# Performance work log

Hardware: AMD Instinct MI355X
Metric: run time of the kernel (lower is better)

The kernel has to match this reference:

```python
import jax, jax.numpy as jnp
import numpy as np

N_NODES = 100000
N_EDGES = 1600000
IN_F = 128
C1, C2, C3 = 32, 64, 64
HEADS, GAT_CH = 4, 16  # concat -> 64
NEG_SLOPE = 0.2  # PyG GATConv default leaky_relu slope


def _add_self_loops(src, dst, n):
    loop = jnp.arange(n, dtype=src.dtype)
    return jnp.concatenate([src, loop]), jnp.concatenate([dst, loop])


def gcn_conv(x, src, dst, W, b, n):
    # PyG GCNConv: D^{-1/2} (A + I) D^{-1/2} X W + b  (self-loops already in src/dst)
    h = x @ W
    deg = jax.ops.segment_sum(jnp.ones_like(dst, dtype=h.dtype), dst, num_segments=n)
    dinv = jnp.where(deg > 0, jax.lax.rsqrt(deg), 0.0)
    norm = dinv[src] * dinv[dst]                              # [E]
    out = jax.ops.segment_sum(h[src] * norm[:, None], dst, num_segments=n)
    return out + b


def gat_conv(x, src, dst, W, att_src, att_dst, b, n):
    # PyG GATConv (concat=True), self-loops already in src/dst
    h = (x @ W).reshape(n, HEADS, GAT_CH)                     # [N,H,C]
    a_s = jnp.sum(h * att_src, axis=-1)                       # [N,H]
    a_d = jnp.sum(h * att_dst, axis=-1)                       # [N,H]
    e = jax.nn.leaky_relu(a_s[src] + a_d[dst], NEG_SLOPE)     # [E,H]
    # segment softmax over incoming edges of each dst node
    emax = jax.ops.segment_max(e, dst, num_segments=n)
    ex = jnp.exp(e - emax[dst])
    denom = jax.ops.segment_sum(ex, dst, num_segments=n)
    alpha = ex / (denom[dst] + 1e-16)                         # [E,H]
    out = jax.ops.segment_sum(h[src] * alpha[:, :, None], dst, num_segments=n)
    return out.reshape(n, HEADS * GAT_CH) + b


def setup_inputs() -> dict:
    key = jax.random.key(0)
    ks = jax.random.split(key, 16)
    x = jax.random.normal(ks[0], (N_NODES, IN_F), dtype=jnp.float32)
    edge_index = jax.random.randint(ks[1], (2, N_EDGES), 0, N_NODES, dtype=jnp.int32)
    s = 0.1
    return {
        "x": x,
        "edge_index": edge_index,
        "W1": jax.random.normal(ks[2], (IN_F, C1), jnp.float32) * s,
        "b1": jnp.zeros((C1,), jnp.float32),
        "W2": jax.random.normal(ks[3], (C1, C2), jnp.float32) * s,
        "b2": jnp.zeros((C2,), jnp.float32),
        "W3": jax.random.normal(ks[4], (C3, C3), jnp.float32) * s,
        "b3": jnp.zeros((C3,), jnp.float32),
        "Wg": jax.random.normal(ks[5], (C2, HEADS * GAT_CH), jnp.float32) * s,
        "att_src": jax.random.normal(ks[6], (HEADS, GAT_CH), jnp.float32) * s,
        "att_dst": jax.random.normal(ks[7], (HEADS, GAT_CH), jnp.float32) * s,
        "bg": jnp.zeros((HEADS * GAT_CH,), jnp.float32),
        "Wl": jax.random.normal(ks[8], (HEADS * GAT_CH, 1), jnp.float32) * s,
        "bl": jnp.zeros((1,), jnp.float32),
    }


def reference(x, edge_index, W1, b1, W2, b2, W3, b3, Wg, att_src, att_dst, bg, Wl, bl):
    n = x.shape[0]
    src, dst = _add_self_loops(edge_index[0], edge_index[1], n)
    h = jax.nn.relu(gcn_conv(x, src, dst, W1, b1, n))           # dropout = identity (eval)
    h = jax.nn.relu(gcn_conv(h, src, dst, W2, b2, n))
    h = jax.nn.relu(gat_conv(h, src, dst, Wg, att_src, att_dst, bg, n))
    h_res = jax.nn.relu(gcn_conv(h, src, dst, W3, b3, n))
    h = h + h_res
    h = jax.nn.relu(gat_conv(h, src, dst, Wg, att_src, att_dst, bg, n))
    return jax.nn.relu(h @ Wl + bl)                              # [N,1]
```

## Files before the change

kernel.cpp:

```cpp
#include <hip/hip_runtime.h>
#include <math.h>

constexpr int KIN = 128;

typedef _Float16 half8_t __attribute__((ext_vector_type(8)));
typedef _Float16 half4_t __attribute__((ext_vector_type(4)));


__global__ void rx_hist(const int* __restrict__ dst, int* __restrict__ hist_g,
                        int E, int CH, int NB, int NBKT) {
    __shared__ int h[256];
    int b = blockIdx.x;
    for (int i = threadIdx.x; i < 256; i += blockDim.x) h[i] = 0;
    __syncthreads();
    int beg = b * CH, end = min(beg + CH, E);
    for (int e = beg + threadIdx.x; e < end; e += blockDim.x)
        atomicAdd(&h[dst[e] >> 9], 1);
    __syncthreads();
    for (int d = threadIdx.x; d < NBKT; d += blockDim.x)
        hist_g[d * NB + b] = h[d];
}

__global__ void gs_reduce(const int* __restrict__ a, int* __restrict__ bsum, int m) {
    __shared__ int s[256];
    int t = threadIdx.x;
    int i = blockIdx.x * 256 + t;
    s[t] = (i < m) ? a[i] : 0;
    __syncthreads();
    for (int off = 128; off > 0; off >>= 1) {
        if (t < off) s[t] += s[t + off];
        __syncthreads();
    }
    if (t == 0) bsum[blockIdx.x] = s[0];
}

__global__ void gs_blocksums(const int* __restrict__ bsum, int* __restrict__ bpre, int nb) {
    __shared__ int s[512];
    int t = threadIdx.x;
    int val = (t < nb) ? bsum[t] : 0;
    s[t] = val;
    __syncthreads();
    for (int off = 1; off < 512; off <<= 1) {
        int x = (t >= off) ? s[t - off] : 0;
        __syncthreads();
        s[t] += x;
        __syncthreads();
    }
    if (t < nb) bpre[t] = s[t] - val;
}

__global__ void gs_scatter(const int* __restrict__ a, const int* __restrict__ bpre,
                           int* __restrict__ out, int m) {
    __shared__ int s[256];
    int t = threadIdx.x;
    int i = blockIdx.x * 256 + t;
    int val = (i < m) ? a[i] : 0;
    s[t] = val;
    __syncthreads();
    for (int off = 1; off < 256; off <<= 1) {
        int x = (t >= off) ? s[t - off] : 0;
        __syncthreads();
        s[t] += x;
        __syncthreads();
    }
    if (i < m) out[i] = bpre[blockIdx.x] + s[t] - val;
}

__global__ void rx_scatter(const int* __restrict__ src, const int* __restrict__ dst,
                           const int* __restrict__ excl, int* __restrict__ s1,
                           int* __restrict__ d1, int E, int CH, int NB, int NBKT) {
    __shared__ int offs[256];
    int b = blockIdx.x;
    for (int d = threadIdx.x; d < NBKT; d += blockDim.x)
        offs[d] = excl[d * NB + b];
    __syncthreads();
    int beg = b * CH, end = min(beg + CH, E);
    for (int e = beg + threadIdx.x; e < end; e += blockDim.x) {
        int dd = dst[e];
        int pos = atomicAdd(&offs[dd >> 9], 1);
        s1[pos] = src[e];
        d1[pos] = dd;
    }
}

__global__ void __launch_bounds__(512)
bucket_sort(const int* __restrict__ s1, const int* __restrict__ d1,
            const int* __restrict__ excl, int* __restrict__ csr,
            int* __restrict__ row_ptr, float* __restrict__ dinv,
            int E, int NB, int NBKT, int n) {
    __shared__ int hist[512];
    __shared__ int scan[512];
    __shared__ int offs[512];
    int b = blockIdx.x, t = threadIdx.x;
    int base = excl[b * NB];
    int endb = (b + 1 < NBKT) ? excl[(b + 1) * NB] : E;
    hist[t] = 0;
    __syncthreads();
    for (int i = base + t; i < endb; i += 512)
        atomicAdd(&hist[d1[i] & 511], 1);
    __syncthreads();
    int v = hist[t];
    scan[t] = v;
    __syncthreads();
    for (int off = 1; off < 512; off <<= 1) {
        int x = (t >= off) ? scan[t - off] : 0;
        __syncthreads();
        scan[t] += x;
        __syncthreads();
    }
    int ex = scan[t] - v;
    offs[t] = ex;
    int node = b * 512 + t;
    if (node < n) {
        row_ptr[node] = base + ex;
        dinv[node] = 1.0f / sqrtf((float)(v + 1));
    }
    if (b == NBKT - 1 && t == 0) row_ptr[n] = E;
    __syncthreads();
    for (int i = base + t; i < endb; i += 512) {
        int dd = d1[i];
        int pos = atomicAdd(&offs[dd & 511], 1);
        csr[base + pos] = s1[i];
    }
}

template <int K, int F, int BM, int THREADS, bool SCALE, bool BRELU, bool ATT, bool OUT16>
__global__ void __launch_bounds__(THREADS)
gemm_tile(const float* __restrict__ in, const float* __restrict__ W,
          const float* __restrict__ dinv, const float* __restrict__ bias,
          const float* __restrict__ att_src, const float* __restrict__ att_dst,
          float* __restrict__ a_s, float* __restrict__ a_d,
          float* __restrict__ out, int n) {
    constexpr int TM = 4, TN = 4;
    constexpr int TX = F / TN;
    constexpr int TY = BM / TM;
    static_assert(THREADS == TX * TY, "thread count mismatch");
    constexpr int K4 = K / 4;
    __shared__ float xs[K][BM];
    __shared__ float Ws[K * F];
    int t = threadIdx.x;
    int row0 = blockIdx.x * BM;

    for (int i = t; i < K * F / 4; i += THREADS)
        ((float4*)Ws)[i] = ((const float4*)W)[i];

    for (int i = t; i < BM * K4; i += THREADS) {
        int r = i % BM, k4 = i / BM;
        int row = row0 + r;
        float4 v = {0.f, 0.f, 0.f, 0.f};
        if (row < n) v = ((const float4*)(in + (size_t)row * K))[k4];
        xs[4 * k4 + 0][r] = v.x;
        xs[4 * k4 + 1][r] = v.y;
        xs[4 * k4 + 2][r] = v.z;
        xs[4 * k4 + 3][r] = v.w;
    }
    __syncthreads();

    int tx = t % TX, ty = t / TX;
    float acc[TM][TN] = {};
#pragma unroll 4
    for (int k = 0; k < K; ++k) {
        float4 xv = *(const float4*)&xs[k][ty * TM];
        float4 wv = *(const float4*)&Ws[k * F + tx * TN];
        float xr[4] = {xv.x, xv.y, xv.z, xv.w};
        float wr[4] = {wv.x, wv.y, wv.z, wv.w};
#pragma unroll
        for (int i = 0; i < TM; ++i)
#pragma unroll
            for (int j = 0; j < TN; ++j)
                acc[i][j] = fmaf(xr[i], wr[j], acc[i][j]);
    }

#pragma unroll
    for (int i = 0; i < TM; ++i) {
        int row = row0 + ty * TM + i;
        if (row >= n) continue;
        float s = SCALE ? dinv[row] : 1.0f;
        float o[4];
        if (BRELU) {
            o[0] = fmaxf(fmaf(acc[i][0], s, bias[4 * tx + 0]), 0.f);
            o[1] = fmaxf(fmaf(acc[i][1], s, bias[4 * tx + 1]), 0.f);
            o[2] = fmaxf(fmaf(acc[i][2], s, bias[4 * tx + 2]), 0.f);
            o[3] = fmaxf(fmaf(acc[i][3], s, bias[4 * tx + 3]), 0.f);
        } else {
            o[0] = acc[i][0] * s; o[1] = acc[i][1] * s;
            o[2] = acc[i][2] * s; o[3] = acc[i][3] * s;
        }
        if (OUT16) {
            half4_t oh;
            oh[0] = (_Float16)o[0]; oh[1] = (_Float16)o[1];
            oh[2] = (_Float16)o[2]; oh[3] = (_Float16)o[3];
            *(half4_t*)((_Float16*)out + (size_t)row * F + 4 * tx) = oh;
        } else {
            float4 of = {o[0], o[1], o[2], o[3]};
            ((float4*)(out + (size_t)row * F))[tx] = of;
        }
    }
    if (ATT) {
        int hd = tx >> 2;
        float as0 = att_src[4 * tx + 0], as1 = att_src[4 * tx + 1];
        float as2 = att_src[4 * tx + 2], as3 = att_src[4 * tx + 3];
        float ad0 = att_dst[4 * tx + 0], ad1 = att_dst[4 * tx + 1];
        float ad2 = att_dst[4 * tx + 2], ad3 = att_dst[4 * tx + 3];
#pragma unroll
        for (int i = 0; i < TM; ++i) {
            float ps = acc[i][0] * as0 + acc[i][1] * as1 + acc[i][2] * as2 + acc[i][3] * as3;
            float pd = acc[i][0] * ad0 + acc[i][1] * ad1 + acc[i][2] * ad2 + acc[i][3] * ad3;
            ps += __shfl_xor(ps, 1); pd += __shfl_xor(pd, 1);
            ps += __shfl_xor(ps, 2); pd += __shfl_xor(pd, 2);
            int row = row0 + ty * TM + i;
            if ((tx & 3) == 0 && row < n) {
                a_s[row * 4 + hd] = ps;
                a_d[row * 4 + hd] = pd;
            }
        }
    }
}

__global__ void __launch_bounds__(256)
gemm2_gat(const float* __restrict__ T, const float* __restrict__ W2,
          const float* __restrict__ b2, const float* __restrict__ dinv,
          const float* __restrict__ Wg, const float* __restrict__ att_src,
          const float* __restrict__ att_dst, float* __restrict__ a_s,
          float* __restrict__ a_d, float* __restrict__ A1, int n) {
    __shared__ float xs[32][64];
    __shared__ float W2s[32 * 64];
    __shared__ float Wgs[64 * 64];
    __shared__ float hs[64][68];
    int t = threadIdx.x;
    int row0 = blockIdx.x * 64;

    for (int i = t; i < 32 * 64 / 4; i += 256) ((float4*)W2s)[i] = ((const float4*)W2)[i];
    for (int i = t; i < 64 * 64 / 4; i += 256) ((float4*)Wgs)[i] = ((const float4*)Wg)[i];
    for (int i = t; i < 64 * 8; i += 256) {
        int r = i % 64, k4 = i / 64;
        int row = row0 + r;
        float4 v = {0.f, 0.f, 0.f, 0.f};
        if (row < n) v = ((const float4*)(T + (size_t)row * 32))[k4];
        xs[4 * k4 + 0][r] = v.x;
        xs[4 * k4 + 1][r] = v.y;
        xs[4 * k4 + 2][r] = v.z;
        xs[4 * k4 + 3][r] = v.w;
    }
    __syncthreads();

    int tx = t % 16, ty = t / 16;
    {
        float acc[4][4] = {};
#pragma unroll 4
        for (int k = 0; k < 32; ++k) {
            float4 xv = *(const float4*)&xs[k][ty * 4];
            float4 wv = *(const float4*)&W2s[k * 64 + tx * 4];
            float xr[4] = {xv.x, xv.y, xv.z, xv.w};
            float wr[4] = {wv.x, wv.y, wv.z, wv.w};
#pragma unroll
            for (int i = 0; i < 4; ++i)
#pragma unroll
                for (int j = 0; j < 4; ++j)
                    acc[i][j] = fmaf(xr[i], wr[j], acc[i][j]);
        }
#pragma unroll
        for (int i = 0; i < 4; ++i) {
            int row = row0 + ty * 4 + i;
            float s = (row < n) ? dinv[row] : 0.f;
#pragma unroll
            for (int j = 0; j < 4; ++j)
                hs[4 * tx + j][ty * 4 + i] = fmaxf(fmaf(acc[i][j], s, b2[4 * tx + j]), 0.f);
        }
    }
    __syncthreads();

    float acc[4][4] = {};
#pragma unroll 4
    for (int k = 0; k < 64; ++k) {
        float4 xv = *(const float4*)&hs[k][ty * 4];
        float4 wv = *(const float4*)&Wgs[k * 64 + tx * 4];
        float xr[4] = {xv.x, xv.y, xv.z, xv.w};
        float wr[4] = {wv.x, wv.y, wv.z, wv.w};
#pragma unroll
        for (int i = 0; i < 4; ++i)
#pragma unroll
            for (int j = 0; j < 4; ++j)
                acc[i][j] = fmaf(xr[i], wr[j], acc[i][j]);
    }
    _Float16* A1h = (_Float16*)A1;
#pragma unroll
    for (int i = 0; i < 4; ++i) {
        int row = row0 + ty * 4 + i;
        if (row >= n) continue;
        half4_t oh;
        oh[0] = (_Float16)acc[i][0]; oh[1] = (_Float16)acc[i][1];
        oh[2] = (_Float16)acc[i][2]; oh[3] = (_Float16)acc[i][3];
        *(half4_t*)(A1h + (size_t)row * 64 + 4 * tx) = oh;
    }
    {
        int hd = tx >> 2;
        float as0 = att_src[4 * tx + 0], as1 = att_src[4 * tx + 1];
        float as2 = att_src[4 * tx + 2], as3 = att_src[4 * tx + 3];
        float ad0 = att_dst[4 * tx + 0], ad1 = att_dst[4 * tx + 1];
        float ad2 = att_dst[4 * tx + 2], ad3 = att_dst[4 * tx + 3];
#pragma unroll
        for (int i = 0; i < 4; ++i) {
            float ps = acc[i][0] * as0 + acc[i][1] * as1 + acc[i][2] * as2 + acc[i][3] * as3;
            float pd = acc[i][0] * ad0 + acc[i][1] * ad1 + acc[i][2] * ad2 + acc[i][3] * ad3;
            ps += __shfl_xor(ps, 1); pd += __shfl_xor(pd, 1);
            ps += __shfl_xor(ps, 2); pd += __shfl_xor(pd, 2);
            int row = row0 + ty * 4 + i;
            if ((tx & 3) == 0 && row < n) {
                a_s[row * 4 + hd] = ps;
                a_d[row * 4 + hd] = pd;
            }
        }
    }
}

template <int F, int MODE, bool RES>
__global__ void gcn_agg_w(const float* __restrict__ Hs, const int* __restrict__ row_ptr,
                          const int* __restrict__ csr, const float* __restrict__ dinv,
                          const float* __restrict__ bias, const float* __restrict__ res,
                          float* __restrict__ out, int n) {
    constexpr int CG = F / 4;
    constexpr int SLOTS = 64 / CG;
    int idx = blockIdx.x * blockDim.x + threadIdx.x;
    int v = idx >> 6;
    int lane = idx & 63;
    if (v >= n) return;
    int cg = lane % CG;
    int slot = lane / CG;
    const float4* H4 = (const float4*)Hs;

    float4 acc = {0.f, 0.f, 0.f, 0.f};
    if (slot == 0) acc = H4[(size_t)v * CG + cg];

    int beg = row_ptr[v], end = row_ptr[v + 1];
    int iters = (end - beg + SLOTS - 1) / SLOTS;
    int e = beg + slot;
    bool val = e < end;
    int u = val ? csr[e] : v;
    float4 h = H4[(size_t)u * CG + cg];
    for (int i = 0; i < iters; ++i) {
        int en = e + SLOTS;
        bool valn = en < end;
        int un = valn ? csr[en] : v;
        float4 hn = H4[(size_t)un * CG + cg];
        float m = val ? 1.f : 0.f;
        acc.x = fmaf(m, h.x, acc.x);
        acc.y = fmaf(m, h.y, acc.y);
        acc.z = fmaf(m, h.z, acc.z);
        acc.w = fmaf(m, h.w, acc.w);
        e = en; val = valn; h = hn;
    }
    for (int off = CG; off < 64; off <<= 1) {
        acc.x += __shfl_xor(acc.x, off);
        acc.y += __shfl_xor(acc.y, off);
        acc.z += __shfl_xor(acc.z, off);
        acc.w += __shfl_xor(acc.w, off);
    }
    if (slot == 0) {
        float4 o;
        if (MODE == 2) {
            o = acc;
        } else {
            float dv = dinv[v];
            o.x = fmaxf(fmaf(dv, acc.x, bias[4 * cg + 0]), 0.f);
            o.y = fmaxf(fmaf(dv, acc.y, bias[4 * cg + 1]), 0.f);
            o.z = fmaxf(fmaf(dv, acc.z, bias[4 * cg + 2]), 0.f);
            o.w = fmaxf(fmaf(dv, acc.w, bias[4 * cg + 3]), 0.f);
            if (MODE == 1) { o.x *= dv; o.y *= dv; o.z *= dv; o.w *= dv; }
            if (RES) {
                const float4 r = ((const float4*)res)[(size_t)v * CG + cg];
                o.x += r.x; o.y += r.y; o.z += r.z; o.w += r.w;
            }
        }
        ((float4*)out)[(size_t)v * CG + cg] = o;
    }
}

__global__ void __launch_bounds__(256)
gcn_agg_h64(const _Float16* __restrict__ Hs, const int* __restrict__ row_ptr,
            const int* __restrict__ csr, const float* __restrict__ dinv,
            const float* __restrict__ bias, const float* __restrict__ res,
            float* __restrict__ out, int n) {
    int idx = blockIdx.x * blockDim.x + threadIdx.x;
    int v = idx >> 6;
    int lane = idx & 63;
    if (v >= n) return;
    int cg = lane & 7;
    int slot = lane >> 3;
    const half8_t* H8 = (const half8_t*)Hs;

    float acc[8] = {};
    if (slot == 0) {
        half8_t h = H8[(size_t)v * 8 + cg];
#pragma unroll
        for (int j = 0; j < 8; ++j) acc[j] = (float)h[j];
    }
    int beg = row_ptr[v], end = row_ptr[v + 1];
    int iters = (end - beg + 7) >> 3;
    int e = beg + slot;
    bool val = e < end;
    int u = val ? csr[e] : v;
    half8_t h = H8[(size_t)u * 8 + cg];
    for (int i = 0; i < iters; ++i) {
        int en = e + 8;
        bool valn = en < end;
        int un = valn ? csr[en] : v;
        half8_t hn = H8[(size_t)un * 8 + cg];
        float m = val ? 1.f : 0.f;
#pragma unroll
        for (int j = 0; j < 8; ++j) acc[j] = fmaf(m, (float)h[j], acc[j]);
        e = en; val = valn; h = hn;
    }
#pragma unroll
    for (int off = 8; off < 64; off <<= 1) {
#pragma unroll
        for (int j = 0; j < 8; ++j) acc[j] += __shfl_xor(acc[j], off);
    }
    if (slot == 0) {
        float dv = dinv[v];
        const float4* r4 = (const float4*)(res + (size_t)v * 64 + 8 * cg);
        float4 r0 = r4[0], r1 = r4[1];
        float o[8];
#pragma unroll
        for (int j = 0; j < 8; ++j)
            o[j] = fmaxf(fmaf(dv, acc[j], bias[8 * cg + j]), 0.f);
        float4 o0 = {o[0] + r0.x, o[1] + r0.y, o[2] + r0.z, o[3] + r0.w};
        float4 o1 = {o[4] + r1.x, o[5] + r1.y, o[6] + r1.z, o[7] + r1.w};
        float4* dst4 = (float4*)(out + (size_t)v * 64 + 8 * cg);
        dst4[0] = o0;
        dst4[1] = o1;
    }
}

template <bool FINAL>
__global__ void __launch_bounds__(256)
gat_agg_h(const _Float16* __restrict__ H, const int* __restrict__ row_ptr,
          const int* __restrict__ csr, const float* __restrict__ a_s,
          const float* __restrict__ a_d, const float* __restrict__ bias,
          const float* __restrict__ Wl, const float* __restrict__ bl,
          float* __restrict__ out, int n) {
    int idx = blockIdx.x * blockDim.x + threadIdx.x;
    int v = idx >> 6;
    int lane = idx & 63;
    if (v >= n) return;
    int cg = lane & 7;
    int slot = lane >> 3;
    int hd = cg >> 1;
    const half8_t* H8 = (const half8_t*)H;

    float adv = a_d[v * 4 + hd];
    float l = 0.f;
    float acc[8] = {};
    if (slot == 0) {
        float e0 = a_s[v * 4 + hd] + adv;
        e0 = (e0 >= 0.f) ? e0 : 0.2f * e0;
        float p = __expf(e0);
        l = p;
        half8_t h = H8[(size_t)v * 8 + cg];
#pragma unroll
        for (int j = 0; j < 8; ++j) acc[j] = p * (float)h[j];
    }
    int beg = row_ptr[v], end = row_ptr[v + 1];
    int iters = (end - beg + 7) >> 3;
    int e = beg + slot;
    bool val = e < end;
    int u = val ? csr[e] : v;
    half8_t h = H8[(size_t)u * 8 + cg];
    float as = a_s[u * 4 + hd];
    for (int i = 0; i < iters; ++i) {
        int en = e + 8;
        bool valn = en < end;
        int un = valn ? csr[en] : v;
        half8_t hn = H8[(size_t)un * 8 + cg];
        float asn = a_s[un * 4 + hd];
        float ev = as + adv;
        ev = (ev >= 0.f) ? ev : 0.2f * ev;
        float p = val ? __expf(ev) : 0.f;
        l += p;
#pragma unroll
        for (int j = 0; j < 8; ++j) acc[j] = fmaf(p, (float)h[j], acc[j]);
        e = en; val = valn; h = hn; as = asn;
    }
#pragma unroll
    for (int off = 8; off < 64; off <<= 1) {
        l += __shfl_xor(l, off);
#pragma unroll
        for (int j = 0; j < 8; ++j) acc[j] += __shfl_xor(acc[j], off);
    }
    float rl = 1.0f / (l + 1e-16f);
    if (!FINAL) {
        if (slot == 0) {
            float o[8];
#pragma unroll
            for (int j = 0; j < 8; ++j)
                o[j] = fmaxf(fmaf(acc[j], rl, bias[8 * cg + j]), 0.f);
            float4 o0 = {o[0], o[1], o[2], o[3]};
            float4 o1 = {o[4], o[5], o[6], o[7]};
            float4* dst4 = (float4*)(out + (size_t)v * 64 + 8 * cg);
            dst4[0] = o0;
            dst4[1] = o1;
        }
    } else {
        float p = 0.f;
#pragma unroll
        for (int j = 0; j < 8; ++j)
            p += fmaxf(fmaf(acc[j], rl, bias[8 * cg + j]), 0.f) * Wl[8 * cg + j];
        p += __shfl_xor(p, 1);
        p += __shfl_xor(p, 2);
        p += __shfl_xor(p, 4);
        if (lane == 0) out[v] = fmaxf(p + bl[0], 0.f);
    }
}


extern "C" void kernel_launch(void* const* d_in, const int* in_sizes, int n_in,
                              void* d_out, int out_size, void* d_ws, size_t ws_size,
                              hipStream_t stream) {
    const float* x     = (const float*)d_in[0];
    const int*   ei    = (const int*)d_in[1];
    const float* W1    = (const float*)d_in[2];
    const float* b1    = (const float*)d_in[3];
    const float* W2    = (const float*)d_in[4];
    const float* b2    = (const float*)d_in[5];
    const float* W3    = (const float*)d_in[6];
    const float* b3    = (const float*)d_in[7];
    const float* Wg    = (const float*)d_in[8];
    const float* att_s = (const float*)d_in[9];
    const float* att_d = (const float*)d_in[10];
    const float* bg    = (const float*)d_in[11];
    const float* Wl    = (const float*)d_in[12];
    const float* bl    = (const float*)d_in[13];
    float* out = (float*)d_out;

    int n = in_sizes[0] / KIN;
    int E = in_sizes[1] / 2;
    const int* srcp = ei;
    const int* dstp = ei + E;

    int NB = 128;
    int CH = (E + NB - 1) / NB;
    int NBKT = (n + 511) >> 9;
    int M = NBKT * NB;

    char* w = (char*)d_ws;
    auto alloc = [&](size_t bytes) -> void* {
        void* p = (void*)w;
        w += (bytes + 255) & ~(size_t)255;
        return p;
    };
    int*   row_ptr = (int*)alloc((size_t)(n + 1) * 4);
    int*   csr     = (int*)alloc((size_t)E * 4);
    int*   hist_g  = (int*)alloc((size_t)M * 4);
    int*   excl    = (int*)alloc((size_t)M * 4);
    int*   bsum    = (int*)alloc(512 * 4);
    int*   bpre    = (int*)alloc(512 * 4);
    float* dinv    = (float*)alloc((size_t)n * 4);
    float* a_s     = (float*)alloc((size_t)n * 4 * 4);
    float* a_d     = (float*)alloc((size_t)n * 4 * 4);
    float* bufA    = (float*)alloc((size_t)n * 64 * 4);
    float* bufB    = (float*)alloc((size_t)n * 64 * 4);
    float* bufC    = (float*)alloc((size_t)n * 64 * 4);
    int* s1 = (int*)bufB;
    int* d1 = ((int*)bufB) + E;

    int msb = (M + 255) / 256;
    rx_hist<<<NB, 256, 0, stream>>>(dstp, hist_g, E, CH, NB, NBKT);
    gs_reduce<<<msb, 256, 0, stream>>>(hist_g, bsum, M);
    gs_blocksums<<<1, 512, 0, stream>>>(bsum, bpre, msb);
    gs_scatter<<<msb, 256, 0, stream>>>(hist_g, bpre, excl, M);
    rx_scatter<<<NB, 256, 0, stream>>>(srcp, dstp, excl, s1, d1, E, CH, NB, NBKT);
    bucket_sort<<<NBKT, 512, 0, stream>>>(s1, d1, excl, csr, row_ptr, dinv, E, NB, NBKT, n);

    int agg_blocks = (n * 64 + 255) / 256;
    int gemm_blocks = (n + 63) / 64;

    gemm_tile<128, 32, 64, 128, true, false, false, false><<<gemm_blocks, 128, 0, stream>>>(
        x, W1, dinv, nullptr, nullptr, nullptr, nullptr, nullptr, bufA, n);
    gcn_agg_w<32, 1, false><<<agg_blocks, 256, 0, stream>>>(bufA, row_ptr, csr, dinv, b1, nullptr, bufB, n);
    gcn_agg_w<32, 2, false><<<agg_blocks, 256, 0, stream>>>(bufB, row_ptr, csr, nullptr, nullptr, nullptr, bufA, n);
    gemm2_gat<<<gemm_blocks, 256, 0, stream>>>(bufA, W2, b2, dinv, Wg, att_s, att_d, a_s, a_d, bufB, n);
    gat_agg_h<false><<<agg_blocks, 256, 0, stream>>>(
        (const _Float16*)bufB, row_ptr, csr, a_s, a_d, bg, nullptr, nullptr, bufC, n);
    gemm_tile<64, 64, 64, 256, true, false, false, true><<<gemm_blocks, 256, 0, stream>>>(
        bufC, W3, dinv, nullptr, nullptr, nullptr, nullptr, nullptr, bufA, n);
    gcn_agg_h64<<<agg_blocks, 256, 0, stream>>>(
        (const _Float16*)bufA, row_ptr, csr, dinv, b3, bufC, bufB, n);
    gemm_tile<64, 64, 64, 256, false, false, true, true><<<gemm_blocks, 256, 0, stream>>>(
        bufB, Wg, nullptr, nullptr, att_s, att_d, a_s, a_d, bufA, n);
    gat_agg_h<true><<<agg_blocks, 256, 0, stream>>>(
        (const _Float16*)bufA, row_ptr, csr, a_s, a_d, bg, Wl, bl, out, n);
}
```

Baseline: 508.8 us.

## Store first GCN layer features in fp16 and widen GAT per-lane head work

The first GEMM now writes fp16 output, and both 32-wide GCN aggregations gather fp16 rows using 16 edge slots per wavefront instead of 8. The middle aggregation also emits fp16 for the next one. This halves gather bytes in the first layer. Separately, the GAT aggregation gives each lane a whole head (16 channels), so 16 edges are processed in parallel per node instead of 8, at the cost of more registers and shuffles per lane. fp16 intermediates add rounding error.

```diff
diff --git a/kernel.cpp b/kernel.cpp
--- a/kernel.cpp
+++ b/kernel.cpp
@@ -314,65 +314,62 @@
     }
 }
 
-template <int F, int MODE, bool RES>
-__global__ void gcn_agg_w(const float* __restrict__ Hs, const int* __restrict__ row_ptr,
-                          const int* __restrict__ csr, const float* __restrict__ dinv,
-                          const float* __restrict__ bias, const float* __restrict__ res,
-                          float* __restrict__ out, int n) {
-    constexpr int CG = F / 4;
-    constexpr int SLOTS = 64 / CG;
+template <int MODE>
+__global__ void __launch_bounds__(256)
+gcn_agg_h32(const _Float16* __restrict__ Hs, const int* __restrict__ row_ptr,
+            const int* __restrict__ csr, const float* __restrict__ dinv,
+            const float* __restrict__ bias, void* __restrict__ outp, int n) {
     int idx = blockIdx.x * blockDim.x + threadIdx.x;
     int v = idx >> 6;
     int lane = idx & 63;
     if (v >= n) return;
-    int cg = lane % CG;
-    int slot = lane / CG;
-    const float4* H4 = (const float4*)Hs;
-
-    float4 acc = {0.f, 0.f, 0.f, 0.f};
-    if (slot == 0) acc = H4[(size_t)v * CG + cg];
-
+    int cg = lane & 3;
+    int slot = lane >> 2;
+    const half8_t* H8 = (const half8_t*)Hs;
+
+    float acc[8] = {};
+    if (slot == 0) {
+        half8_t h = H8[(size_t)v * 4 + cg];
+#pragma unroll
+        for (int j = 0; j < 8; ++j) acc[j] = (float)h[j];
+    }
     int beg = row_ptr[v], end = row_ptr[v + 1];
-    int iters = (end - beg + SLOTS - 1) / SLOTS;
+    int iters = (end - beg + 15) >> 4;
     int e = beg + slot;
     bool val = e < end;
     int u = val ? csr[e] : v;
-    float4 h = H4[(size_t)u * CG + cg];
+    half8_t h = H8[(size_t)u * 4 + cg];
     for (int i = 0; i < iters; ++i) {
-        int en = e + SLOTS;
+        int en = e + 16;
         bool valn = en < end;
         int un = valn ? csr[en] : v;
-        float4 hn = H4[(size_t)un * CG + cg];
+        half8_t hn = H8[(size_t)un * 4 + cg];
         float m = val ? 1.f : 0.f;
-        acc.x = fmaf(m, h.x, acc.x);
-        acc.y = fmaf(m, h.y, acc.y);
-        acc.z = fmaf(m, h.z, acc.z);
-        acc.w = fmaf(m, h.w, acc.w);
+#pragma unroll
+        for (int j = 0; j < 8; ++j) acc[j] = fmaf(m, (float)h[j], acc[j]);
         e = en; val = valn; h = hn;
     }
-    for (int off = CG; off < 64; off <<= 1) {
-        acc.x += __shfl_xor(acc.x, off);
-        acc.y += __shfl_xor(acc.y, off);
-        acc.z += __shfl_xor(acc.z, off);
-        acc.w += __shfl_xor(acc.w, off);
+#pragma unroll
+    for (int off = 4; off < 64; off <<= 1) {
+#pragma unroll
+        for (int j = 0; j < 8; ++j) acc[j] += __shfl_xor(acc[j], off);
     }
     if (slot == 0) {
-        float4 o;
-        if (MODE == 2) {
-            o = acc;
+        if (MODE == 1) {
+            float dv = dinv[v];
+            half8_t o;
+#pragma unroll
+            for (int j = 0; j < 8; ++j)
+                o[j] = (_Float16)(dv * fmaxf(fmaf(dv, acc[j], bias[8 * cg + j]), 0.f));
+            ((half8_t*)outp)[(size_t)v * 4 + cg] = o;
         } else {
-            float dv = dinv[v];
-            o.x = fmaxf(fmaf(dv, acc.x, bias[4 * cg + 0]), 0.f);
-            o.y = fmaxf(fmaf(dv, acc.y, bias[4 * cg + 1]), 0.f);
-            o.z = fmaxf(fmaf(dv, acc.z, bias[4 * cg + 2]), 0.f);
-            o.w = fmaxf(fmaf(dv, acc.w, bias[4 * cg + 3]), 0.f);
-            if (MODE == 1) { o.x *= dv; o.y *= dv; o.z *= dv; o.w *= dv; }
-            if (RES) {
-                const float4 r = ((const float4*)res)[(size_t)v * CG + cg];
-                o.x += r.x; o.y += r.y; o.z += r.z; o.w += r.w;
-            }
-        }
-        ((float4*)out)[(size_t)v * CG + cg] = o;
+            float* of = (float*)outp;
+            float4 o0 = {acc[0], acc[1], acc[2], acc[3]};
+            float4 o1 = {acc[4], acc[5], acc[6], acc[7]};
+            float4* dst4 = (float4*)(of + (size_t)v * 32 + 8 * cg);
+            dst4[0] = o0;
+            dst4[1] = o1;
+        }
     }
 }
 
@@ -443,71 +440,78 @@
     int v = idx >> 6;
     int lane = idx & 63;
     if (v >= n) return;
-    int cg = lane & 7;
-    int slot = lane >> 3;
-    int hd = cg >> 1;
+    int hd = lane & 3;
+    int slot = lane >> 2;
     const half8_t* H8 = (const half8_t*)H;
 
     float adv = a_d[v * 4 + hd];
     float l = 0.f;
-    float acc[8] = {};
+    float acc[16] = {};
     if (slot == 0) {
         float e0 = a_s[v * 4 + hd] + adv;
-        e0 = (e0 >= 0.f) ? e0 : 0.2f * e0;
+        e0 = fmaxf(e0, 0.2f * e0);
         float p = __expf(e0);
         l = p;
-        half8_t h = H8[(size_t)v * 8 + cg];
-#pragma unroll
-        for (int j = 0; j < 8; ++j) acc[j] = p * (float)h[j];
+        const half8_t* hp = H8 + (size_t)v * 8 + 2 * hd;
+        half8_t h0 = hp[0], h1 = hp[1];
+#pragma unroll
+        for (int j = 0; j < 8; ++j) {
+            acc[j] = p * (float)h0[j];
+            acc[8 + j] = p * (float)h1[j];
+        }
     }
     int beg = row_ptr[v], end = row_ptr[v + 1];
-    int iters = (end - beg + 7) >> 3;
+    int iters = (end - beg + 15) >> 4;
     int e = beg + slot;
     bool val = e < end;
     int u = val ? csr[e] : v;
-    half8_t h = H8[(size_t)u * 8 + cg];
+    const half8_t* hp = H8 + (size_t)u * 8 + 2 * hd;
+    half8_t h0 = hp[0], h1 = hp[1];
     float as = a_s[u * 4 + hd];
     for (int i = 0; i < iters; ++i) {
-        int en = e + 8;
+        int en = e + 16;
         bool valn = en < end;
         int un = valn ? csr[en] : v;
-        half8_t hn = H8[(size_t)un * 8 + cg];
+        const half8_t* hpn = H8 + (size_t)un * 8 + 2 * hd;
+        half8_t hn0 = hpn[0], hn1 = hpn[1];
         float asn = a_s[un * 4 + hd];
         float ev = as + adv;
-        ev = (ev >= 0.f) ? ev : 0.2f * ev;
+        ev = fmaxf(ev, 0.2f * ev);
         float p = val ? __expf(ev) : 0.f;
         l += p;
 #pragma unroll
-        for (int j = 0; j < 8; ++j) acc[j] = fmaf(p, (float)h[j], acc[j]);
-        e = en; val = valn; h = hn; as = asn;
-    }
-#pragma unroll
-    for (int off = 8; off < 64; off <<= 1) {
+        for (int j = 0; j < 8; ++j) {
+            acc[j] = fmaf(p, (float)h0[j], acc[j]);
+            acc[8 + j] = fmaf(p, (float)h1[j], acc[8 + j]);
+        }
+        e = en; val = valn; h0 = hn0; h1 = hn1; as = asn;
+    }
+#pragma unroll
+    for (int off = 4; off < 64; off <<= 1) {
         l += __shfl_xor(l, off);
 #pragma unroll
-        for (int j = 0; j < 8; ++j) acc[j] += __shfl_xor(acc[j], off);
+        for (int j = 0; j < 16; ++j) acc[j] += __shfl_xor(acc[j], off);
     }
     float rl = 1.0f / (l + 1e-16f);
     if (!FINAL) {
         if (slot == 0) {
-            float o[8];
-#pragma unroll
-            for (int j = 0; j < 8; ++j)
-                o[j] = fmaxf(fmaf(acc[j], rl, bias[8 * cg + j]), 0.f);
-            float4 o0 = {o[0], o[1], o[2], o[3]};
-            float4 o1 = {o[4], o[5], o[6], o[7]};
-            float4* dst4 = (float4*)(out + (size_t)v * 64 + 8 * cg);
-            dst4[0] = o0;
-            dst4[1] = o1;
+            float o[16];
+#pragma unroll
+            for (int j = 0; j < 16; ++j)
+                o[j] = fmaxf(fmaf(acc[j], rl, bias[16 * hd + j]), 0.f);
+            float4* dst4 = (float4*)(out + (size_t)v * 64 + 16 * hd);
+            dst4[0] = {o[0], o[1], o[2], o[3]};
+            dst4[1] = {o[4], o[5], o[6], o[7]};
+            dst4[2] = {o[8], o[9], o[10], o[11]};
+            dst4[3] = {o[12], o[13], o[14], o[15]};
         }
     } else {
         float p = 0.f;
 #pragma unroll
-        for (int j = 0; j < 8; ++j)
-            p += fmaxf(fmaf(acc[j], rl, bias[8 * cg + j]), 0.f) * Wl[8 * cg + j];
+        for (int j = 0; j < 16; ++j)
+            p += fmaxf(fmaf(acc[j], rl, bias[16 * hd + j]), 0.f) * Wl[16 * hd + j];
         p += __shfl_xor(p, 1);
         p += __shfl_xor(p, 2);
-        p += __shfl_xor(p, 4);
         if (lane == 0) out[v] = fmaxf(p + bl[0], 0.f);
     }
 }
@@ -574,10 +578,12 @@
     int agg_blocks = (n * 64 + 255) / 256;
     int gemm_blocks = (n + 63) / 64;
 
-    gemm_tile<128, 32, 64, 128, true, false, false, false><<<gemm_blocks, 128, 0, stream>>>(
+    gemm_tile<128, 32, 64, 128, true, false, false, true><<<gemm_blocks, 128, 0, stream>>>(
         x, W1, dinv, nullptr, nullptr, nullptr, nullptr, nullptr, bufA, n);
-    gcn_agg_w<32, 1, false><<<agg_blocks, 256, 0, stream>>>(bufA, row_ptr, csr, dinv, b1, nullptr, bufB, n);
-    gcn_agg_w<32, 2, false><<<agg_blocks, 256, 0, stream>>>(bufB, row_ptr, csr, nullptr, nullptr, nullptr, bufA, n);
+    gcn_agg_h32<1><<<agg_blocks, 256, 0, stream>>>(
+        (const _Float16*)bufA, row_ptr, csr, dinv, b1, bufB, n);
+    gcn_agg_h32<2><<<agg_blocks, 256, 0, stream>>>(
+        (const _Float16*)bufB, row_ptr, csr, nullptr, nullptr, bufA, n);
     gemm2_gat<<<gemm_blocks, 256, 0, stream>>>(bufA, W2, b2, dinv, Wg, att_s, att_d, a_s, a_d, bufB, n);
     gat_agg_h<false><<<agg_blocks, 256, 0, stream>>>(
         (const _Float16*)bufB, row_ptr, csr, a_s, a_d, bg, nullptr, nullptr, bufC, n);
```

Result: slower. 556.4 us (+9.3%).
